# Optimization experiments

Hardware: AMD Instinct MI355X
Metric: run time of the kernel (lower is better)

## Reference

```python
import jax, jax.numpy as jnp
import numpy as np

B, S, D, H = 2, 2048, 1024, 16
HD = D // H               # head_dim = input_size / num_heads
STEPS = 1                 # update_steps_max extra Hopfield update steps
LN_EPS = 1e-5
SCALING = 1.0 / np.sqrt(HD)  # beta = 1/sqrt(head_dim)


def layernorm(x, g, b):
    m = x.mean(-1, keepdims=True)
    v = ((x - m) ** 2).mean(-1, keepdims=True)
    return (x - m) * jax.lax.rsqrt(v + LN_EPS) * g + b


def setup_inputs() -> dict:
    key = jax.random.key(0)
    ks = jax.random.split(key, 9)
    s = 0.02
    f32 = jnp.float32
    return {
        "data": jax.random.normal(ks[0], (B, S, D), f32),
        # affine LayerNorm params (stored / state / projection patterns)
        "g_k": jnp.ones((D,), f32), "b_k": jnp.zeros((D,), f32),
        "g_q": jnp.ones((D,), f32), "b_q": jnp.zeros((D,), f32),
        "g_v": jnp.ones((D,), f32), "b_v": jnp.zeros((D,), f32),
        # in-projections (q/k/v) and out-projection of HopfieldCore
        "Wq": jax.random.normal(ks[1], (D, D), f32) * s, "bq": jnp.zeros((D,), f32),
        "Wk": jax.random.normal(ks[2], (D, D), f32) * s, "bk": jnp.zeros((D,), f32),
        "Wv": jax.random.normal(ks[3], (D, D), f32) * s, "bv": jnp.zeros((D,), f32),
        "Wo": jax.random.normal(ks[4], (D, D), f32) * s, "bo": jnp.zeros((D,), f32),
    }


def reference(data, g_k, b_k, g_q, b_q, g_v, b_v,
              Wq, bq, Wk, bk, Wv, bv, Wo, bo):
    # single input tensor used as stored / state / projection pattern
    xk = layernorm(data, g_k, b_k)   # stored pattern  -> keys
    xq = layernorm(data, g_q, b_q)   # state pattern   -> queries
    xv = layernorm(data, g_v, b_v)   # pattern proj    -> values

    split = lambda t: t.reshape(B, S, H, HD).transpose(0, 2, 1, 3)  # [B,H,S,HD]
    q = split(xq @ Wq + bq)
    k = split(xk @ Wk + bk)
    v = split(xv @ Wv + bv)

    def assoc(q):  # xi = softmax(beta * q K^T)
        return jax.nn.softmax(
            jnp.einsum('bhqd,bhkd->bhqk', q, k) * SCALING, axis=-1)

    xi = assoc(q)
    for _ in range(STEPS):           # iterative Hopfield update: q <- xi K
        q = jnp.einsum('bhqk,bhkd->bhqd', xi, k)
        xi = assoc(q)

    out = jnp.einsum('bhqk,bhkd->bhqd', xi, v)        # retrieve with values
    out = out.transpose(0, 2, 1, 3).reshape(B, S, D)  # merge heads
    return out @ Wo + bo
```

## Files before the change

kernel.cpp:

```cpp
#include <hip/hip_runtime.h>
#include <hip/hip_bf16.h>

#define B_  2
#define S_  2048
#define D_  1024
#define H_  16
#define HD_ 64
#define M_  4096


typedef __attribute__((ext_vector_type(8))) short short8;
typedef __attribute__((ext_vector_type(4))) float f32x4;
typedef __attribute__((ext_vector_type(2))) float f32x2;
typedef __attribute__((ext_vector_type(16))) float f32x16;

#define CE_ 0.1803368801111204f

typedef __attribute__((address_space(1))) const unsigned GU;
typedef __attribute__((address_space(3))) unsigned LU;
static __device__ __forceinline__ void glds16(const void* g, void* l){
  __builtin_amdgcn_global_load_lds((GU*)g, (LU*)l, 16, 0, 0);
}

static __device__ __forceinline__ unsigned short f2bfc(float f){
  union{float f; unsigned u;} c; c.f = f;
  return (unsigned short)((c.u + 0x8000u) >> 16);
}
static __device__ __forceinline__ unsigned pk2bf(float a, float b){
  union{float f; unsigned u;} ca, cb; ca.f=a; cb.f=b;
  return __builtin_amdgcn_perm(cb.u + 0x8000u, ca.u + 0x8000u, 0x07060302u);
}
static __device__ __forceinline__ unsigned pk2bft(float a, float b){
  union{float f; unsigned u;} ca, cb; ca.f=a; cb.f=b;
  return __builtin_amdgcn_perm(cb.u, ca.u, 0x07060302u);
}
static __device__ __forceinline__ short8 mk8(unsigned x0, unsigned x1,
                                             unsigned x2, unsigned x3){
  union{ unsigned u[4]; short8 s; } t;
  t.u[0]=x0; t.u[1]=x1; t.u[2]=x2; t.u[3]=x3; return t.s;
}
static __device__ __forceinline__ void plswap(unsigned &x, unsigned &y){
  auto r = __builtin_amdgcn_permlane32_swap(x, y, false, false);
  x = (unsigned)r[0]; y = (unsigned)r[1];
}
static __device__ __forceinline__ short8 conv8a(const f32x16& v, float iv){
  unsigned a0 = pk2bf(v[0]*iv, v[1]*iv);
  unsigned a1 = pk2bf(v[2]*iv, v[3]*iv);
  unsigned b0 = pk2bf(v[4]*iv, v[5]*iv);
  unsigned b1 = pk2bf(v[6]*iv, v[7]*iv);
  plswap(a0,b0); plswap(a1,b1);
  return mk8(a0,a1,b0,b1);
}
static __device__ __forceinline__ short8 conv8b(const f32x16& v, float iv){
  unsigned a0 = pk2bf(v[8]*iv,  v[9]*iv);
  unsigned a1 = pk2bf(v[10]*iv, v[11]*iv);
  unsigned b0 = pk2bf(v[12]*iv, v[13]*iv);
  unsigned b1 = pk2bf(v[14]*iv, v[15]*iv);
  plswap(a0,b0); plswap(a1,b1);
  return mk8(a0,a1,b0,b1);
}

__global__ __launch_bounds__(256) void prep_kernel(
  const float* __restrict__ data,
  const float* __restrict__ Wq, const float* __restrict__ Wk,
  const float* __restrict__ Wv, const float* __restrict__ Wo,
  const float* __restrict__ gq, const float* __restrict__ gk, const float* __restrict__ gv,
  const float* __restrict__ blq, const float* __restrict__ blk, const float* __restrict__ blv,
  const float* __restrict__ bpq, const float* __restrict__ bpk, const float* __restrict__ bpv,
  unsigned short* __restrict__ WT, unsigned short* __restrict__ xhat,
  float* __restrict__ bf)
{
  __shared__ unsigned short tile[64][72];
  __shared__ float red[4][64];
  int bid = blockIdx.x, t = threadIdx.x;
  if (bid < 1024){
    int z = bid >> 8, rem = bid & 255;
    int k0 = (rem>>4)*64, n0 = (rem&15)*64;
    const float* W = (z==0)?Wq:(z==1)?Wk:(z==2)?Wv:Wo;
    const float* g = (z==0)?gq:(z==1)?gk:(z==2)?gv:(const float*)0;
    unsigned short* out = WT + ((size_t)z<<20);
    {
      int kr = t>>2, c16 = (t&3)*16;
      float gs = g ? g[k0+kr]*((z==0)?CE_:1.0f) : 1.0f;
      const float* src = W + (size_t)(k0+kr)*D_ + n0 + c16;
      float4 w0 = *(const float4*)(src);
      float4 w1 = *(const float4*)(src+4);
      float4 w2 = *(const float4*)(src+8);
      float4 w3 = *(const float4*)(src+12);
      unsigned* tp = (unsigned*)&tile[kr][c16];
      tp[0]=pk2bf(w0.x*gs,w0.y*gs); tp[1]=pk2bf(w0.z*gs,w0.w*gs);
      tp[2]=pk2bf(w1.x*gs,w1.y*gs); tp[3]=pk2bf(w1.z*gs,w1.w*gs);
      tp[4]=pk2bf(w2.x*gs,w2.y*gs); tp[5]=pk2bf(w2.z*gs,w2.w*gs);
      tp[6]=pk2bf(w3.x*gs,w3.y*gs); tp[7]=pk2bf(w3.z*gs,w3.w*gs);
    }
    __syncthreads();
    {
      int nr = t>>2, kc = (t&3)*16;
      union { uint4 v[2]; unsigned short u[16]; } st;
      #pragma unroll
      for (int i=0;i<16;i++) st.u[i] = tile[kc+i][nr];
      unsigned short* dst = out + (size_t)(n0+nr)*D_ + k0 + kc;
      *(uint4*)(dst)     = st.v[0];
      *(uint4*)(dst + 8) = st.v[1];
    }
  } else if (bid < 2048){
    int row = (bid-1024)*4 + (t>>6);
    int l = t & 63;
    const float4* xr = (const float4*)(data + (size_t)row*D_);
    float4 v[4];
    float s = 0.f, ss = 0.f;
    #pragma unroll
    for (int i=0;i<4;i++){
      v[i] = xr[l + 64*i];
      s  += v[i].x+v[i].y+v[i].z+v[i].w;
      ss += v[i].x*v[i].x+v[i].y*v[i].y+v[i].z*v[i].z+v[i].w*v[i].w;
    }
    #pragma unroll
    for (int m=1;m<64;m<<=1){ s += __shfl_xor(s, m, 64); ss += __shfl_xor(ss, m, 64); }
    float me = s*(1.0f/D_);
    float var = ss*(1.0f/D_) - me*me;
    float rs = rsqrtf(var + 1e-5f);
    float nm = -me*rs;
    unsigned short* xo = xhat + (size_t)row*D_;
    #pragma unroll
    for (int i=0;i<4;i++){
      uint2 pk;
      pk.x = pk2bf(fmaf(v[i].x,rs,nm), fmaf(v[i].y,rs,nm));
      pk.y = pk2bf(fmaf(v[i].z,rs,nm), fmaf(v[i].w,rs,nm));
      *(uint2*)(xo + 4*l + 256*i) = pk;
    }
  } else {
    int idx = bid - 2048;
    int z = idx >> 4, xb = idx & 15;
    const float* W  = (z==0)?Wq:(z==1)?Wk:Wv;
    const float* bl = (z==0)?blq:(z==1)?blk:blv;
    const float* bp = (z==0)?bpq:(z==1)?bpk:bpv;
    int nl = t & 63, kg = t >> 6;
    int n = xb*64 + nl;
    float acc = 0.f;
    for (int k = kg*256; k < (kg+1)*256; k++)
      acc += bl[k] * W[(size_t)k*D_ + n];
    red[kg][nl] = acc;
    __syncthreads();
    if (t < 64){
      int nn = xb*64 + t;
      float v = red[0][t]+red[1][t]+red[2][t]+red[3][t] + bp[nn];
      bf[z*D_ + nn] = (z==0) ? v*CE_ : v;
    }
  }
}

__global__ __launch_bounds__(256) void gemm_qkv(
  const unsigned short* __restrict__ xhat,
  const unsigned short* __restrict__ WT,
  const float* __restrict__ biasf,
  unsigned short* __restrict__ qv, unsigned short* __restrict__ kb,
  unsigned short* __restrict__ kT, unsigned short* __restrict__ vT)
{
  int z = blockIdx.z;
  const unsigned short* Bt = WT + ((size_t)z<<20);
  const float* bias = biasf + z*D_;
  unsigned short* oN = (z==0)?qv:(z==1)?kb:(unsigned short*)0;
  unsigned short* oT = (z==0)?(unsigned short*)0:(z==1)?kT:vT;

  __shared__ __align__(16) unsigned short smem[8704];
  unsigned short* As = smem;
  unsigned short* Bs = smem + 4096;
  int tid = threadIdx.x, w = tid>>6, l = tid&63;
  int m0 = blockIdx.x*128, n0 = blockIdx.y*64;
  int wr = (w>>1)*64, wc = (w&1)*32;
  int lr = l&15, qd = l>>4;

  const unsigned short* gA = xhat + (size_t)(m0 + w*32 + (l>>2))*D_ + (l&3)*8;
  const unsigned short* gB = Bt   + (size_t)(n0 + w*16 + (l>>2))*D_ + (l&3)*8;
  unsigned short* lA0 = &As[(w*32)*32];
  unsigned short* lA1 = &As[(w*32+16)*32];
  unsigned short* lB0 = &Bs[(w*16)*32];

  const f32x4 fz = {0.f,0.f,0.f,0.f};
  f32x4 acc[4][2];
  #pragma unroll
  for (int i=0;i<4;i++)
    #pragma unroll
    for (int j=0;j<2;j++) acc[i][j] = fz;

  for (int kk=0; kk<D_; kk+=32){
    __syncthreads();
    glds16(gA + kk,                 lA0);
    glds16(gA + kk + (size_t)16*D_, lA1);
    glds16(gB + kk,                 lB0);
    __syncthreads();
    short8 af[4], bfr[2];
    #pragma unroll
    for (int i=0;i<4;i++) af[i]  = *(const short8*)(As + (wr + i*16 + lr)*32 + qd*8);
    #pragma unroll
    for (int j=0;j<2;j++) bfr[j] = *(const short8*)(Bs + (wc + j*16 + lr)*32 + qd*8);
    #pragma unroll
    for (int i=0;i<4;i++)
      #pragma unroll
      for (int j=0;j<2;j++)
        acc[i][j] = __builtin_amdgcn_mfma_f32_16x16x32_bf16(af[i], bfr[j], acc[i][j], 0, 0, 0);
  }

  if (oN){
    #pragma unroll
    for (int j=0;j<2;j++){
      int n = n0 + wc + j*16 + lr;
      float bias_n = bias[n];
      #pragma unroll
      for (int i=0;i<4;i++){
        int mb = m0 + wr + i*16 + qd*4;
        oN[(size_t)(mb+0)*D_ + n] = f2bfc(acc[i][j][0] + bias_n);
        oN[(size_t)(mb+1)*D_ + n] = f2bfc(acc[i][j][1] + bias_n);
        oN[(size_t)(mb+2)*D_ + n] = f2bfc(acc[i][j][2] + bias_n);
        oN[(size_t)(mb+3)*D_ + n] = f2bfc(acc[i][j][3] + bias_n);
      }
    }
  }
  if (oT){
    __syncthreads();
    #pragma unroll
    for (int j=0;j<2;j++){
      int nl_ = wc + j*16 + lr;
      float bias_n = bias[n0 + nl_];
      #pragma unroll
      for (int i=0;i<4;i++){
        int ml_ = wr + i*16 + qd*4;
        uint2 pk;
        pk.x = pk2bf(acc[i][j][0] + bias_n, acc[i][j][1] + bias_n);
        pk.y = pk2bf(acc[i][j][2] + bias_n, acc[i][j][3] + bias_n);
        *(uint2*)(smem + nl_*136 + ml_) = pk;
      }
    }
    __syncthreads();
    int bb = m0 >> 11;
    int s0 = m0 & (S_-1);
    int hh = n0 >> 6;
    int dl = tid >> 4;
    int ml = (tid & 15) * 8;
    #pragma unroll
    for (int p=0;p<4;p++){
      int dd = p*16 + dl;
      uint4 vv = *(const uint4*)(smem + dd*136 + ml);
      *(uint4*)(oT + (size_t)((bb*H_ + hh)*HD_ + dd)*S_ + (s0 + ml)) = vv;
    }
  }
}

__global__ __launch_bounds__(256) void gemm_out(
  const unsigned short* __restrict__ A,
  const unsigned short* __restrict__ Bt,
  const float* __restrict__ bo,
  float* __restrict__ Cf)
{
  __shared__ __align__(16) unsigned short As[128*32];
  __shared__ __align__(16) unsigned short Bs[64*32];
  int tid = threadIdx.x, w = tid>>6, l = tid&63;
  int m0 = blockIdx.x*128, n0 = blockIdx.y*64;
  int wr = (w>>1)*64, wc = (w&1)*32;
  int lr = l&15, qd = l>>4;

  const unsigned short* gA = A  + (size_t)(m0 + w*32 + (l>>2))*D_ + (l&3)*8;
  const unsigned short* gB = Bt + (size_t)(n0 + w*16 + (l>>2))*D_ + (l&3)*8;
  unsigned short* lA0 = &As[(w*32)*32];
  unsigned short* lA1 = &As[(w*32+16)*32];
  unsigned short* lB0 = &Bs[(w*16)*32];

  const f32x4 fz = {0.f,0.f,0.f,0.f};
  f32x4 acc[4][2];
  #pragma unroll
  for (int i=0;i<4;i++)
    #pragma unroll
    for (int j=0;j<2;j++) acc[i][j] = fz;

  for (int kk=0; kk<D_; kk+=32){
    __syncthreads();
    glds16(gA + kk,                 lA0);
    glds16(gA + kk + (size_t)16*D_, lA1);
    glds16(gB + kk,                 lB0);
    __syncthreads();
    short8 af[4], bfr[2];
    #pragma unroll
    for (int i=0;i<4;i++) af[i]  = *(const short8*)(As + (wr + i*16 + lr)*32 + qd*8);
    #pragma unroll
    for (int j=0;j<2;j++) bfr[j] = *(const short8*)(Bs + (wc + j*16 + lr)*32 + qd*8);
    #pragma unroll
    for (int i=0;i<4;i++)
      #pragma unroll
      for (int j=0;j<2;j++)
        acc[i][j] = __builtin_amdgcn_mfma_f32_16x16x32_bf16(af[i], bfr[j], acc[i][j], 0, 0, 0);
  }

  #pragma unroll
  for (int j=0;j<2;j++){
    int n = n0 + wc + j*16 + lr;
    float bias_n = bo[n];
    #pragma unroll
    for (int i=0;i<4;i++){
      int mb = m0 + wr + i*16 + qd*4;
      Cf[(size_t)(mb+0)*D_ + n] = acc[i][j][0] + bias_n;
      Cf[(size_t)(mb+1)*D_ + n] = acc[i][j][1] + bias_n;
      Cf[(size_t)(mb+2)*D_ + n] = acc[i][j][2] + bias_n;
      Cf[(size_t)(mb+3)*D_ + n] = acc[i][j][3] + bias_n;
    }
  }
}

__global__ __launch_bounds__(256, 4) void attn_fused(
  unsigned short* __restrict__ QO,
  const unsigned short* __restrict__ K,
  const unsigned short* __restrict__ KT,
  const unsigned short* __restrict__ VT)
{
  int lin = blockIdx.x + (blockIdx.y << 6);
  int id  = ((lin & 7) << 7) + (lin >> 3);
  int qt = id & 63;
  int h  = id >> 6;
  int b  = qt >> 5;
  int bh = b*H_ + h;
  int tid = threadIdx.x, w = tid>>6, l = tid&63;
  int wq = w & 1, wk = w >> 1;
  int lq = l & 31, hi = l >> 5;
  int swzr = (lq & 7) << 3;

  __shared__ __align__(16) unsigned short smem[17408];

  const f32x16 fz16 = {0.f,0.f,0.f,0.f,0.f,0.f,0.f,0.f,
                       0.f,0.f,0.f,0.f,0.f,0.f,0.f,0.f};

  const unsigned short* Qb = QO + (size_t)(qt*64 + wq*32 + lq)*D_ + h*64;
  short8 qf[4];
  #pragma unroll
  for (int d=0; d<4; d++) qf[d] = *(const short8*)(Qb + d*16 + hi*8);

  const unsigned short* Khead = K + (size_t)(b*S_)*D_ + h*64;
  const unsigned short* Vh0 = KT + (size_t)bh*HD_*S_;
  const unsigned short* Vh1 = VT + (size_t)bh*HD_*S_;

  int seg0 = w*2;
  int lr8 = l>>3;
  int swzs = ((l&7)*8) ^ (lr8*8);
  const unsigned short* gKs  = Khead + (size_t)(seg0*8 + lr8)*D_ + swzs;
  const unsigned short* gV0s = Vh0 + (size_t)(seg0*8 + lr8)*S_ + swzs;
  const unsigned short* gV1s = Vh1 + (size_t)(seg0*8 + lr8)*S_ + swzs;
  int dK0 = seg0*512 + l*8;
  int dV0 = 4096 + seg0*512 + l*8;

  glds16(gKs,         smem + dK0);
  glds16(gKs + 8*D_,  smem + dK0 + 512);
  glds16(gV0s,        smem + dV0);
  glds16(gV0s + 8*S_, smem + dV0 + 512);
  __syncthreads();

  #pragma unroll 1
  for (int phase=0; phase<2; phase++){
    f32x16 oacc[2]; oacc[0]=fz16; oacc[1]=fz16;
    f32x2 dq = {0.f,0.f};

    #pragma unroll 1
    for (int ss=0; ss<32; ss++){
      int t = phase*32 + ss;
      if (t < 63){
        int tn = t + 1;
        int tt = tn & 31;
        unsigned short* bb = smem + ((tn&1) ? 8192 : 0);
        const unsigned short* gk = gKs + (size_t)tt*64*D_;
        const unsigned short* gv = ((tn >= 32) ? gV1s : gV0s) + tt*64;
        glds16(gk,         bb + dK0);
        glds16(gk + 8*D_,  bb + dK0 + 512);
        glds16(gv,         bb + dV0);
        glds16(gv + 8*S_,  bb + dV0 + 512);
      }
      __builtin_amdgcn_sched_barrier(0);

      const unsigned short* sKc = smem + ((t&1) ? 8192 : 0);
      const unsigned short* sVc = sKc + 4096;

      f32x16 sc = fz16;
      __builtin_amdgcn_s_setprio(1);
      #pragma unroll
      for (int d4=0; d4<4; d4++){
        short8 ka = *(const short8*)(sKc + (size_t)(wk*32 + lq)*64 + ((d4*16 + hi*8) ^ swzr));
        sc = __builtin_amdgcn_mfma_f32_32x32x16_bf16(ka, qf[d4], sc, 0,0,0);
      }
      __builtin_amdgcn_s_setprio(0);

      #pragma unroll
      for (int i=0;i<16;i++) sc[i] = __builtin_amdgcn_exp2f(sc[i]);
      #pragma unroll
      for (int i=0;i<16;i+=2) dq += (f32x2){sc[i], sc[i+1]};

      short8 pf[2];
      {
        unsigned a0,a1,b0,b1;
        a0=pk2bft(sc[0],sc[1]);   a1=pk2bft(sc[2],sc[3]);
        b0=pk2bft(sc[4],sc[5]);   b1=pk2bft(sc[6],sc[7]);
        plswap(a0,b0); plswap(a1,b1);
        pf[0] = mk8(a0,a1,b0,b1);
        a0=pk2bft(sc[8],sc[9]);   a1=pk2bft(sc[10],sc[11]);
        b0=pk2bft(sc[12],sc[13]); b1=pk2bft(sc[14],sc[15]);
        plswap(a0,b0); plswap(a1,b1);
        pf[1] = mk8(a0,a1,b0,b1);
      }

      __builtin_amdgcn_s_setprio(1);
      #pragma unroll
      for (int dr=0; dr<2; dr++){
        #pragma unroll
        for (int ks=0; ks<2; ks++){
          short8 va = *(const short8*)(sVc + (size_t)(dr*32 + lq)*64 + ((wk*32 + ks*16 + hi*8) ^ swzr));
          oacc[dr] = __builtin_amdgcn_mfma_f32_32x32x16_bf16(va, pf[ks], oacc[dr], 0,0,0);
        }
      }
      __builtin_amdgcn_s_setprio(0);

      __syncthreads();
    }

    float den = dq.x + dq.y;
    den += __shfl_xor(den, 32, 64);

    float* fb  = (float*)(smem + 8192);
    float* dnp = (float*)(smem + 16384);
    if (wk==1){
      #pragma unroll
      for (int dr=0; dr<2; dr++)
        #pragma unroll
        for (int g=0; g<16; g++)
          fb[wq*2048 + (dr*16+g)*64 + l] = oacc[dr][g];
      dnp[wq*64 + l] = den;
    }
    __syncthreads();
    if (wk==0){
      #pragma unroll
      for (int dr=0; dr<2; dr++)
        #pragma unroll
        for (int g=0; g<16; g++)
          oacc[dr][g] += fb[wq*2048 + (dr*16+g)*64 + l];
      den += dnp[wq*64 + l];
      if (phase==0){
        float iv = CE_ * __builtin_amdgcn_rcpf(den);
        qf[0] = conv8a(oacc[0], iv);
        qf[1] = conv8b(oacc[0], iv);
        qf[2] = conv8a(oacc[1], iv);
        qf[3] = conv8b(oacc[1], iv);
        unsigned short* qsh = smem + 8192 + wq*6144;
        #pragma unroll
        for (int d=0; d<4; d++)
          *(short8*)(qsh + d*512 + l*8) = qf[d];
      } else {
        float iv = __builtin_amdgcn_rcpf(den);
        unsigned short* Ob = QO + (size_t)(qt*64 + wq*32 + lq)*D_ + h*64 + hi*4;
        #pragma unroll
        for (int g=0; g<4; g++){
          uint2 pk;
          pk.x = pk2bf(oacc[0][4*g+0]*iv, oacc[0][4*g+1]*iv);
          pk.y = pk2bf(oacc[0][4*g+2]*iv, oacc[0][4*g+3]*iv);
          *(uint2*)(Ob + g*8) = pk;
          pk.x = pk2bf(oacc[1][4*g+0]*iv, oacc[1][4*g+1]*iv);
          pk.y = pk2bf(oacc[1][4*g+2]*iv, oacc[1][4*g+3]*iv);
          *(uint2*)(Ob + 32 + g*8) = pk;
        }
      }
    }
    __syncthreads();
    if (phase==0 && wk==1){
      unsigned short* qsh = smem + 8192 + wq*6144;
      #pragma unroll
      for (int d=0; d<4; d++)
        qf[d] = *(const short8*)(qsh + d*512 + l*8);
    }
    __syncthreads();
  }
}

extern "C" void kernel_launch(void* const* d_in, const int* in_sizes, int n_in,
                              void* d_out, int out_size, void* d_ws, size_t ws_size,
                              hipStream_t stream){
  const float* data = (const float*)d_in[0];
  const float* g_k  = (const float*)d_in[1];
  const float* b_k  = (const float*)d_in[2];
  const float* g_q  = (const float*)d_in[3];
  const float* b_q  = (const float*)d_in[4];
  const float* g_v  = (const float*)d_in[5];
  const float* b_v  = (const float*)d_in[6];
  const float* Wq   = (const float*)d_in[7];
  const float* bq   = (const float*)d_in[8];
  const float* Wk   = (const float*)d_in[9];
  const float* bk   = (const float*)d_in[10];
  const float* Wv   = (const float*)d_in[11];
  const float* bv   = (const float*)d_in[12];
  const float* Wo   = (const float*)d_in[13];
  const float* bo   = (const float*)d_in[14];
  float* out = (float*)d_out;

  char* ws = (char*)d_ws;
  const size_t MB = (size_t)1<<20;
  unsigned short* q    = (unsigned short*)(ws);
  unsigned short* kb   = (unsigned short*)(ws + 8*MB);
  unsigned short* WT   = (unsigned short*)(ws + 16*MB);
  unsigned short* WTo  = WT + ((size_t)3<<20);
  unsigned short* xhat = (unsigned short*)(ws + 24*MB);
  float*          bfld = (float*)(ws + 32*MB);
  unsigned short* vT   = (unsigned short*)d_out;
  unsigned short* kT   = (unsigned short*)((char*)d_out + 8*MB);

  dim3 gb(256);
  prep_kernel<<<dim3(2096), gb, 0, stream>>>(data,
                                             Wq, Wk, Wv, Wo, g_q, g_k, g_v,
                                             b_q, b_k, b_v, bq, bk, bv,
                                             WT, xhat, bfld);
  gemm_qkv<<<dim3(32,16,3), gb, 0, stream>>>(xhat, WT, bfld, q, kb, kT, vT);
  attn_fused<<<dim3(64, H_), gb, 0, stream>>>(q, kb, kT, vT);
  gemm_out<<<dim3(32,16), gb, 0, stream>>>(q, WTo, bo, out);
}
```

Before: 250.9 us.

## Fuse Q/K/V projections into one block sharing the A tile

Each block now computes the Q, K and V projections for the same 128x64 output tile. One xhat A tile is loaded per k-step and reused across three weight tiles, so A traffic drops to a third and each barrier covers three times as many MFMAs. The grid is flattened to 512 blocks with a swizzled block-to-tile mapping, and launch bounds ask for 2 blocks per CU. The cost is three times the accumulator registers (96 floats per lane), which may cause spills and lower occupancy, and a longer serial epilogue.

```diff
diff --git a/kernel.cpp b/kernel.cpp
--- a/kernel.cpp
+++ b/kernel.cpp
@@ -150,100 +150,138 @@
   }
 }
 
-__global__ __launch_bounds__(256) void gemm_qkv(
+__global__ __launch_bounds__(256, 2) void gemm_qkv(
   const unsigned short* __restrict__ xhat,
   const unsigned short* __restrict__ WT,
   const float* __restrict__ biasf,
   unsigned short* __restrict__ qv, unsigned short* __restrict__ kb,
   unsigned short* __restrict__ kT, unsigned short* __restrict__ vT)
 {
-  int z = blockIdx.z;
-  const unsigned short* Bt = WT + ((size_t)z<<20);
-  const float* bias = biasf + z*D_;
-  unsigned short* oN = (z==0)?qv:(z==1)?kb:(unsigned short*)0;
-  unsigned short* oT = (z==0)?(unsigned short*)0:(z==1)?kT:vT;
-
-  __shared__ __align__(16) unsigned short smem[8704];
+  int id = blockIdx.x;
+  int slot = id >> 3;
+  int by = ((id & 7) << 1) | (slot & 1);
+  int bx = slot >> 1;
+  int m0 = bx*128, n0 = by*64;
+  int hh = by;
+
+  __shared__ __align__(16) unsigned short smem[10240];
   unsigned short* As = smem;
-  unsigned short* Bs = smem + 4096;
   int tid = threadIdx.x, w = tid>>6, l = tid&63;
-  int m0 = blockIdx.x*128, n0 = blockIdx.y*64;
   int wr = (w>>1)*64, wc = (w&1)*32;
   int lr = l&15, qd = l>>4;
 
-  const unsigned short* gA = xhat + (size_t)(m0 + w*32 + (l>>2))*D_ + (l&3)*8;
-  const unsigned short* gB = Bt   + (size_t)(n0 + w*16 + (l>>2))*D_ + (l&3)*8;
+  const unsigned short* gA  = xhat + (size_t)(m0 + w*32 + (l>>2))*D_ + (l&3)*8;
+  const unsigned short* gB0 = WT   + (size_t)(n0 + w*16 + (l>>2))*D_ + (l&3)*8;
+  const unsigned short* gB1 = gB0 + ((size_t)1<<20);
+  const unsigned short* gB2 = gB0 + ((size_t)2<<20);
   unsigned short* lA0 = &As[(w*32)*32];
   unsigned short* lA1 = &As[(w*32+16)*32];
-  unsigned short* lB0 = &Bs[(w*16)*32];
+  unsigned short* lB0 = smem + 4096 + (w*16)*32;
+  unsigned short* lB1 = lB0 + 2048;
+  unsigned short* lB2 = lB0 + 4096;
 
   const f32x4 fz = {0.f,0.f,0.f,0.f};
-  f32x4 acc[4][2];
-  #pragma unroll
-  for (int i=0;i<4;i++)
-    #pragma unroll
-    for (int j=0;j<2;j++) acc[i][j] = fz;
+  f32x4 acc[3][4][2];
+  #pragma unroll
+  for (int z=0;z<3;z++)
+    #pragma unroll
+    for (int i=0;i<4;i++)
+      #pragma unroll
+      for (int j=0;j<2;j++) acc[z][i][j] = fz;
 
   for (int kk=0; kk<D_; kk+=32){
     __syncthreads();
-    glds16(gA + kk,                 lA0);
-    glds16(gA + kk + (size_t)16*D_, lA1);
-    glds16(gB + kk,                 lB0);
-    __syncthreads();
-    short8 af[4], bfr[2];
+    glds16(gA  + kk,                 lA0);
+    glds16(gA  + kk + (size_t)16*D_, lA1);
+    glds16(gB0 + kk, lB0);
+    glds16(gB1 + kk, lB1);
+    glds16(gB2 + kk, lB2);
+    __syncthreads();
+    short8 af[4], bf0[2], bf1[2], bf2[2];
     #pragma unroll
     for (int i=0;i<4;i++) af[i]  = *(const short8*)(As + (wr + i*16 + lr)*32 + qd*8);
     #pragma unroll
-    for (int j=0;j<2;j++) bfr[j] = *(const short8*)(Bs + (wc + j*16 + lr)*32 + qd*8);
+    for (int j=0;j<2;j++){
+      int off = (wc + j*16 + lr)*32 + qd*8;
+      bf0[j] = *(const short8*)(smem + 4096 + off);
+      bf1[j] = *(const short8*)(smem + 6144 + off);
+      bf2[j] = *(const short8*)(smem + 8192 + off);
+    }
     #pragma unroll
     for (int i=0;i<4;i++)
       #pragma unroll
-      for (int j=0;j<2;j++)
-        acc[i][j] = __builtin_amdgcn_mfma_f32_16x16x32_bf16(af[i], bfr[j], acc[i][j], 0, 0, 0);
-  }
-
-  if (oN){
-    #pragma unroll
-    for (int j=0;j<2;j++){
-      int n = n0 + wc + j*16 + lr;
-      float bias_n = bias[n];
-      #pragma unroll
-      for (int i=0;i<4;i++){
-        int mb = m0 + wr + i*16 + qd*4;
-        oN[(size_t)(mb+0)*D_ + n] = f2bfc(acc[i][j][0] + bias_n);
-        oN[(size_t)(mb+1)*D_ + n] = f2bfc(acc[i][j][1] + bias_n);
-        oN[(size_t)(mb+2)*D_ + n] = f2bfc(acc[i][j][2] + bias_n);
-        oN[(size_t)(mb+3)*D_ + n] = f2bfc(acc[i][j][3] + bias_n);
+      for (int j=0;j<2;j++){
+        acc[0][i][j] = __builtin_amdgcn_mfma_f32_16x16x32_bf16(af[i], bf0[j], acc[0][i][j], 0, 0, 0);
+        acc[1][i][j] = __builtin_amdgcn_mfma_f32_16x16x32_bf16(af[i], bf1[j], acc[1][i][j], 0, 0, 0);
+        acc[2][i][j] = __builtin_amdgcn_mfma_f32_16x16x32_bf16(af[i], bf2[j], acc[2][i][j], 0, 0, 0);
       }
-    }
-  }
-  if (oT){
-    __syncthreads();
-    #pragma unroll
-    for (int j=0;j<2;j++){
-      int nl_ = wc + j*16 + lr;
-      float bias_n = bias[n0 + nl_];
-      #pragma unroll
-      for (int i=0;i<4;i++){
-        int ml_ = wr + i*16 + qd*4;
-        uint2 pk;
-        pk.x = pk2bf(acc[i][j][0] + bias_n, acc[i][j][1] + bias_n);
-        pk.y = pk2bf(acc[i][j][2] + bias_n, acc[i][j][3] + bias_n);
-        *(uint2*)(smem + nl_*136 + ml_) = pk;
-      }
-    }
-    __syncthreads();
-    int bb = m0 >> 11;
-    int s0 = m0 & (S_-1);
-    int hh = n0 >> 6;
-    int dl = tid >> 4;
-    int ml = (tid & 15) * 8;
-    #pragma unroll
-    for (int p=0;p<4;p++){
-      int dd = p*16 + dl;
-      uint4 vv = *(const uint4*)(smem + dd*136 + ml);
-      *(uint4*)(oT + (size_t)((bb*H_ + hh)*HD_ + dd)*S_ + (s0 + ml)) = vv;
-    }
+  }
+
+  #pragma unroll
+  for (int j=0;j<2;j++){
+    int n = n0 + wc + j*16 + lr;
+    float b0 = biasf[n];
+    float b1 = biasf[D_ + n];
+    #pragma unroll
+    for (int i=0;i<4;i++){
+      int mb = m0 + wr + i*16 + qd*4;
+      qv[(size_t)(mb+0)*D_ + n] = f2bfc(acc[0][i][j][0] + b0);
+      qv[(size_t)(mb+1)*D_ + n] = f2bfc(acc[0][i][j][1] + b0);
+      qv[(size_t)(mb+2)*D_ + n] = f2bfc(acc[0][i][j][2] + b0);
+      qv[(size_t)(mb+3)*D_ + n] = f2bfc(acc[0][i][j][3] + b0);
+      kb[(size_t)(mb+0)*D_ + n] = f2bfc(acc[1][i][j][0] + b1);
+      kb[(size_t)(mb+1)*D_ + n] = f2bfc(acc[1][i][j][1] + b1);
+      kb[(size_t)(mb+2)*D_ + n] = f2bfc(acc[1][i][j][2] + b1);
+      kb[(size_t)(mb+3)*D_ + n] = f2bfc(acc[1][i][j][3] + b1);
+    }
+  }
+
+  int bb = m0 >> 11;
+  int s0 = m0 & (S_-1);
+  int dl = tid >> 4;
+  int ml = (tid & 15) * 8;
+
+  __syncthreads();
+  #pragma unroll
+  for (int j=0;j<2;j++){
+    int nl_ = wc + j*16 + lr;
+    float bn = biasf[D_ + n0 + nl_];
+    #pragma unroll
+    for (int i=0;i<4;i++){
+      int ml_ = wr + i*16 + qd*4;
+      uint2 pk;
+      pk.x = pk2bf(acc[1][i][j][0] + bn, acc[1][i][j][1] + bn);
+      pk.y = pk2bf(acc[1][i][j][2] + bn, acc[1][i][j][3] + bn);
+      *(uint2*)(smem + nl_*136 + ml_) = pk;
+    }
+  }
+  __syncthreads();
+  #pragma unroll
+  for (int p=0;p<4;p++){
+    int dd = p*16 + dl;
+    uint4 vv = *(const uint4*)(smem + dd*136 + ml);
+    *(uint4*)(kT + (size_t)((bb*H_ + hh)*HD_ + dd)*S_ + (s0 + ml)) = vv;
+  }
+  __syncthreads();
+  #pragma unroll
+  for (int j=0;j<2;j++){
+    int nl_ = wc + j*16 + lr;
+    float bn = biasf[2*D_ + n0 + nl_];
+    #pragma unroll
+    for (int i=0;i<4;i++){
+      int ml_ = wr + i*16 + qd*4;
+      uint2 pk;
+      pk.x = pk2bf(acc[2][i][j][0] + bn, acc[2][i][j][1] + bn);
+      pk.y = pk2bf(acc[2][i][j][2] + bn, acc[2][i][j][3] + bn);
+      *(uint2*)(smem + nl_*136 + ml_) = pk;
+    }
+  }
+  __syncthreads();
+  #pragma unroll
+  for (int p=0;p<4;p++){
+    int dd = p*16 + dl;
+    uint4 vv = *(const uint4*)(smem + dd*136 + ml);
+    *(uint4*)(vT + (size_t)((bb*H_ + hh)*HD_ + dd)*S_ + (s0 + ml)) = vv;
   }
 }
 
@@ -510,7 +548,7 @@
                                              Wq, Wk, Wv, Wo, g_q, g_k, g_v,
                                              b_q, b_k, b_v, bq, bk, bv,
                                              WT, xhat, bfld);
-  gemm_qkv<<<dim3(32,16,3), gb, 0, stream>>>(xhat, WT, bfld, q, kb, kT, vT);
+  gemm_qkv<<<dim3(512), gb, 0, stream>>>(xhat, WT, bfld, q, kb, kT, vT);
   attn_fused<<<dim3(64, H_), gb, 0, stream>>>(q, kb, kT, vT);
   gemm_out<<<dim3(32,16), gb, 0, stream>>>(q, WTo, bo, out);
 }
```

After: 245.9 us. 2.0% less time.
